# Performance work log

Hardware: AMD Instinct MI355X
Metric: run time of the kernel (lower is better)

## Reference

```python
import jax, jax.numpy as jnp
import numpy as np

B, T, F, C, L, W, NT, H = 4096, 64, 32, 64, 256, 512, 8, 12

# Tsit5 Butcher tableau (fixed-step, 6-stage FSAL-free form)
A21 = 0.161
A31, A32 = -0.008480655492356989, 0.335480655492357
A41, A42, A43 = 2.8971530571054935, -6.359448489975075, 4.362295432869581
A51, A52, A53, A54 = 5.325864828439257, -11.748883564062828, 7.4955393428898365, -0.09249506636175525
A61, A62, A63, A64, A65 = 5.86145544294642, -12.92096931784711, 8.159367898576159, -0.071584973281401, -0.028269050394068383
BC1, BC2, BC3, BC4, BC5, BC6 = 0.09646076681806523, 0.01, 0.4798896504144996, 1.379008574103742, -3.290069515436081, 2.324710524099774
SUBSTEPS = 10  # dt0 = 0.1, integrate each unit interval with 10 fixed steps


def setup_inputs() -> dict:
    key = jax.random.key(0)
    ks = jax.random.split(key, 16)
    def lin(k, out_d, in_d, scale=None):
        s = (1.0 / np.sqrt(in_d)) if scale is None else scale
        return jax.random.normal(k, (out_d, in_d), jnp.float32) * s
    inp = {
        "x_seq": jax.random.normal(ks[0], (B, T, F), jnp.float32),
        "country_idx": jax.random.randint(ks[1], (B,), 0, C),
        "horizon": H,
        # GRU encoder params (equinox GRUCell layout: 3*hidden stacked r,z,n)
        "W_ih": lin(ks[2], 3 * L, F + C),
        "W_hh": lin(ks[3], 3 * L, L),
        "b_ih": jnp.zeros((3 * L,), jnp.float32),
        "b_n": jnp.zeros((L,), jnp.float32),
        # NeuralField MLP 256->512->512->256, small init to keep the ODE stable
        "W0": lin(ks[4], W, L, 0.1 / np.sqrt(L)),
        "b0": jnp.zeros((W,), jnp.float32),
        "W1": lin(ks[5], W, W, 0.1 / np.sqrt(W)),
        "b1": jnp.zeros((W,), jnp.float32),
        "W2": lin(ks[6], L, W, 0.1 / np.sqrt(W)),
        "b2": jnp.zeros((L,), jnp.float32),
        # Decoder
        "W_dec": lin(ks[7], NT, L),
        "b_dec": jnp.zeros((NT,), jnp.float32),
    }
    return inp


def reference(x_seq, W_ih, W_hh, b_ih, b_n, W0, b0, W1, b1, W2, b2, W_dec, b_dec, country_idx, horizon):
    dtype = x_seq.dtype
    n_countries = W_ih.shape[1] - x_seq.shape[2]
    n_latent = W_hh.shape[1]
    ohe = jax.nn.one_hot(country_idx, n_countries, dtype=dtype)  # [B, C]

    # ---- GRU encoder scan over time ----
    h0 = jnp.zeros((x_seq.shape[0], n_latent), dtype)
    def gru_step(h, x_t):
        x_in = jnp.concatenate([x_t, ohe], axis=-1)          # [B, F+C]
        ih = x_in @ W_ih.T + b_ih                            # [B, 3L]
        hh = h @ W_hh.T                                      # [B, 3L]
        ir, iz, inn = jnp.split(ih, 3, axis=-1)
        hr, hz, hn = jnp.split(hh, 3, axis=-1)
        r = jax.nn.sigmoid(ir + hr)
        z = jax.nn.sigmoid(iz + hz)
        n = jnp.tanh(inn + r * (hn + b_n))
        return n + z * (h - n), None
    h_final, _ = jax.lax.scan(gru_step, h0, jnp.swapaxes(x_seq, 0, 1))

    # ---- Neural ODE vector field (autonomous ELU MLP) ----
    def f(y):
        a = jax.nn.elu(y @ W0.T + b0)
        a = jax.nn.elu(a @ W1.T + b1)
        return a @ W2.T + b2

    dt = jnp.asarray(1.0 / SUBSTEPS, dtype)
    def tsit5_step(y, _):
        k1 = f(y)
        k2 = f(y + dt * (A21 * k1))
        k3 = f(y + dt * (A31 * k1 + A32 * k2))
        k4 = f(y + dt * (A41 * k1 + A42 * k2 + A43 * k3))
        k5 = f(y + dt * (A51 * k1 + A52 * k2 + A53 * k3 + A54 * k4))
        k6 = f(y + dt * (A61 * k1 + A62 * k2 + A63 * k3 + A64 * k4 + A65 * k5))
        y_new = y + dt * (BC1 * k1 + BC2 * k2 + BC3 * k3 + BC4 * k4 + BC5 * k5 + BC6 * k6)
        return y_new, None

    def unit(y, _):
        y, _ = jax.lax.scan(tsit5_step, y, None, length=SUBSTEPS)
        return y, y  # save state at each integer time t = 1..horizon

    _, ys = jax.lax.scan(unit, h_final, None, length=horizon)  # [H, B, L]

    # ---- linear decode ----
    out = jnp.einsum('hbl,tl->bht', ys, W_dec) + b_dec  # [B, H, n_targets]
    return out
```

## Files before the change

### kernel.cpp

```cpp
#include <hip/hip_runtime.h>

typedef __bf16 bf16;
typedef __bf16 bf16x8 __attribute__((ext_vector_type(8)));
typedef __bf16 bf16x4 __attribute__((ext_vector_type(4)));
typedef float  f32x4  __attribute__((ext_vector_type(4)));
typedef unsigned int u32;

#define B_TOT 4096
#define T_SEQ 64
#define NT_OUT 8
#define NTHR 512
#define NBLK 256
#define GSZ  8

#define WS_W0   0
#define WS_W1   262144
#define WS_W2   786432
#define WS_WHH  1048576
#define WS_WIH  1441792
#define WS_BC   1490944
#define WS_GY   1703936
#define WS_GYB  3801088
#define WS_GH1  5898240
#define WS_GH2  10092544
#define WS_FLG  14286848
#define WS_MAP  14290944

constexpr float A21 = 0.161f;
constexpr float A31 = -0.008480655492356989f, A32 = 0.335480655492357f;
constexpr float A41 = 2.8971530571054935f, A42 = -6.359448489975075f, A43 = 4.362295432869581f;
constexpr float A51 = 5.325864828439257f, A52 = -11.748883564062828f, A53 = 7.4955393428898365f, A54 = -0.09249506636175525f;
constexpr float A61 = 5.86145544294642f, A62 = -12.92096931784711f, A63 = 8.159367898576159f, A64 = -0.071584973281401f, A65 = -0.028269050394068383f;
constexpr float BC1 = 0.09646076681806523f, BC2 = 0.01f, BC3 = 0.4798896504144996f;
constexpr float BC4 = 1.379008574103742f, BC5 = -3.290069515436081f, BC6 = 2.324710524099774f;
constexpr float DT = 0.1f;
constexpr float BROW[5][5] = {
    {A21, 0, 0, 0, 0},
    {A31, A32, 0, 0, 0},
    {A41, A42, A43, 0, 0},
    {A51, A52, A53, A54, 0},
    {A61, A62, A63, A64, A65}};
constexpr float FCF[6] = {BC1, BC2, BC3, BC4, BC5, BC6};

__device__ __forceinline__ f32x4 MFMA(bf16x8 a, bf16x8 b, f32x4 c) {
    return __builtin_amdgcn_mfma_f32_16x16x32_bf16(a, b, c, 0, 0, 0);
}
__device__ __forceinline__ float eluf(float x) { return x > 0.f ? x : __expf(x) - 1.f; }
__device__ __forceinline__ float sigm_f(float x) { return 1.f / (1.f + __expf(-x)); }
__device__ __forceinline__ float tanh_f(float x) { return 1.f - 2.f / (__expf(2.f * x) + 1.f); }

template<bool FAST>
__device__ __forceinline__ void ld4g(const bf16* p, bf16x8& a0, bf16x8& a1, bf16x8& a2, bf16x8& a3) {
    if constexpr (FAST) {
        asm volatile(
            "global_load_dwordx4 %0, %4, off sc0\n\t"
            "global_load_dwordx4 %1, %4, off offset:1024 sc0\n\t"
            "global_load_dwordx4 %2, %4, off offset:2048 sc0\n\t"
            "global_load_dwordx4 %3, %4, off offset:3072 sc0"
            : "=&v"(a0), "=&v"(a1), "=&v"(a2), "=&v"(a3) : "v"(p) : "memory");
    } else {
        asm volatile(
            "global_load_dwordx4 %0, %4, off sc0 sc1\n\t"
            "global_load_dwordx4 %1, %4, off offset:1024 sc0 sc1\n\t"
            "global_load_dwordx4 %2, %4, off offset:2048 sc0 sc1\n\t"
            "global_load_dwordx4 %3, %4, off offset:3072 sc0 sc1"
            : "=&v"(a0), "=&v"(a1), "=&v"(a2), "=&v"(a3) : "v"(p) : "memory");
    }
}
template<bool FAST>
__device__ __forceinline__ bf16x8 ld1g(const bf16* p) {
    bf16x8 a;
    if constexpr (FAST)
        asm volatile("global_load_dwordx4 %0, %1, off sc0\n\ts_waitcnt vmcnt(0)"
                     : "=v"(a) : "v"(p) : "memory");
    else
        asm volatile("global_load_dwordx4 %0, %1, off sc0 sc1\n\ts_waitcnt vmcnt(0)"
                     : "=v"(a) : "v"(p) : "memory");
    return a;
}
template<bool FAST>
__device__ __forceinline__ void st4g(bf16* p, bf16x4 v) {
    if constexpr (FAST) *(bf16x4*)p = v;
    else asm volatile("global_store_dwordx2 %0, %1, off sc0 sc1" :: "v"(p), "v"(v) : "memory");
}
__device__ __forceinline__ void vmwait() {
    asm volatile("s_waitcnt vmcnt(0)" ::: "memory");
    __builtin_amdgcn_sched_barrier(0);
}

__device__ __forceinline__ void produce(u32* f, int tid) {
    asm volatile("s_waitcnt vmcnt(0)" ::: "memory");
    __syncthreads();
    if (tid == 0) __hip_atomic_fetch_add(f, 1u, __ATOMIC_RELAXED, __HIP_MEMORY_SCOPE_AGENT);
}
__device__ __forceinline__ void consume(const u32* f, u32 tgt, int tid) {
    if (tid == 0) {
        while (__hip_atomic_load(f, __ATOMIC_RELAXED, __HIP_MEMORY_SCOPE_AGENT) < tgt)
            __builtin_amdgcn_s_sleep(1);
    }
    __syncthreads();
}

template<int ST, bool FAST>
__device__ __forceinline__ void ode_stage(
    const bf16* sW0, const bf16* sW1, const bf16* sW2,
    bf16* gY, bf16* gH1, bf16* gH2,
    u32* fY, u32* fH1, u32* fH2, int tid, int w, int lane,
    const f32x4 (&b0v)[4], const f32x4 (&b1v)[4], const f32x4 (&b2v)[2],
    const int (&dA)[4], const int (&dY)[2],
    f32x4 (&yreg)[2], f32x4 (&kreg)[5][2],
    u32& eY, u32& eH1, u32& eH2) {
    const f32x4 Z = {0.f, 0.f, 0.f, 0.f};
    {
        bf16x8 a[8];
        const bf16* p = gY + w * 4096 + lane * 8;
        ld4g<FAST>(p, a[0], a[1], a[2], a[3]);
        ld4g<FAST>(p + 2048, a[4], a[5], a[6], a[7]);
        vmwait();
        f32x4 acc[4] = {Z, Z, Z, Z};
        #pragma unroll
        for (int kk = 0; kk < 8; ++kk)
            #pragma unroll
            for (int nt = 0; nt < 4; ++nt)
                acc[nt] = MFMA(*(const bf16x8*)&sW0[(nt * 8 + kk) * 512 + lane * 8], a[kk], acc[nt]);
        #pragma unroll
        for (int nt = 0; nt < 4; ++nt) {
            bf16x4 ov;
            #pragma unroll
            for (int r = 0; r < 4; ++r) ov[r] = (bf16)eluf(acc[nt][r] + b0v[nt][r]);
            st4g<FAST>(gH1 + w * 8192 + dA[nt], ov);
        }
    }
    produce(fH1, tid); ++eH1;
    consume(fH1, GSZ * eH1, tid);
    {
        bf16x8 a[16];
        const bf16* p = gH1 + w * 8192 + lane * 8;
        ld4g<FAST>(p, a[0], a[1], a[2], a[3]);
        ld4g<FAST>(p + 2048, a[4], a[5], a[6], a[7]);
        ld4g<FAST>(p + 4096, a[8], a[9], a[10], a[11]);
        ld4g<FAST>(p + 6144, a[12], a[13], a[14], a[15]);
        vmwait();
        f32x4 acc[4] = {Z, Z, Z, Z};
        #pragma unroll
        for (int kk = 0; kk < 16; ++kk)
            #pragma unroll
            for (int nt = 0; nt < 4; ++nt)
                acc[nt] = MFMA(*(const bf16x8*)&sW1[(nt * 16 + kk) * 512 + lane * 8], a[kk], acc[nt]);
        #pragma unroll
        for (int nt = 0; nt < 4; ++nt) {
            bf16x4 ov;
            #pragma unroll
            for (int r = 0; r < 4; ++r) ov[r] = (bf16)eluf(acc[nt][r] + b1v[nt][r]);
            st4g<FAST>(gH2 + w * 8192 + dA[nt], ov);
        }
    }
    produce(fH2, tid); ++eH2;
    consume(fH2, GSZ * eH2, tid);
    {
        bf16x8 a[16];
        const bf16* p = gH2 + w * 8192 + lane * 8;
        ld4g<FAST>(p, a[0], a[1], a[2], a[3]);
        ld4g<FAST>(p + 2048, a[4], a[5], a[6], a[7]);
        ld4g<FAST>(p + 4096, a[8], a[9], a[10], a[11]);
        ld4g<FAST>(p + 6144, a[12], a[13], a[14], a[15]);
        vmwait();
        f32x4 acc[2] = {Z, Z};
        #pragma unroll
        for (int kk = 0; kk < 16; ++kk)
            #pragma unroll
            for (int nt = 0; nt < 2; ++nt)
                acc[nt] = MFMA(*(const bf16x8*)&sW2[(nt * 16 + kk) * 512 + lane * 8], a[kk], acc[nt]);
        #pragma unroll
        for (int nt = 0; nt < 2; ++nt) {
            f32x4 kv;
            #pragma unroll
            for (int r = 0; r < 4; ++r) kv[r] = acc[nt][r] + b2v[nt][r];
            f32x4 yst;
            if constexpr (ST < 5) {
                kreg[ST][nt] = kv;
                yst = yreg[nt];
                #pragma unroll
                for (int s = 0; s <= ST; ++s) {
                    const float c = DT * BROW[ST][s];
                    #pragma unroll
                    for (int r = 0; r < 4; ++r) yst[r] += c * kreg[s][nt][r];
                }
            } else {
                #pragma unroll
                for (int s = 0; s < 5; ++s) {
                    const float c = DT * FCF[s];
                    #pragma unroll
                    for (int r = 0; r < 4; ++r) yreg[nt][r] += c * kreg[s][nt][r];
                }
                #pragma unroll
                for (int r = 0; r < 4; ++r) yreg[nt][r] += (DT * FCF[5]) * kv[r];
                yst = yreg[nt];
            }
            bf16x4 ov;
            #pragma unroll
            for (int r = 0; r < 4; ++r) ov[r] = (bf16)yst[r];
            st4g<FAST>(gY + w * 4096 + dY[nt], ov);
        }
    }
    produce(fY, tid); ++eY;
}

template<bool FAST>
__device__ __forceinline__ void dec_unit(const bf16* gY, const float* sWdec, const float* sBdec,
                                         float* out, int g, int j, int w, int lane, int H, int u) {
    const int rloc = 2 * w + (lane >> 5);
    const int li = lane & 31;
    const bf16* p = gY + (size_t)j * 4096 + (((li >> 2) * 64 + (li & 3) * 16 + rloc)) * 8;
    bf16x8 yv = ld1g<FAST>(p);
    const int f0 = li * 8;
    float acc[8];
    #pragma unroll
    for (int t = 0; t < 8; ++t) acc[t] = 0.f;
    #pragma unroll
    for (int e = 0; e < 8; ++e) {
        const float yf = (float)yv[e];
        #pragma unroll
        for (int t = 0; t < 8; ++t) acc[t] += yf * sWdec[t * 256 + f0 + e];
    }
    #pragma unroll
    for (int k = 1; k < 32; k <<= 1)
        #pragma unroll
        for (int t = 0; t < 8; ++t) acc[t] += __shfl_xor(acc[t], k, 64);
    if (li == 0) {
        const size_t row = (size_t)g * 128 + 16 * j + rloc;
        #pragma unroll
        for (int t = 0; t < 8; ++t) out[(row * H + u) * NT_OUT + t] = acc[t] + sBdec[t];
    }
}

template<bool FAST>
__device__ void body(const float* __restrict__ x_seq, const int* __restrict__ cidx,
                     const float* __restrict__ b_n, const float* __restrict__ b0,
                     const float* __restrict__ b1, const float* __restrict__ b2,
                     const float* __restrict__ W_dec, const float* __restrict__ b_dec,
                     char* __restrict__ ws, float* __restrict__ out,
                     bf16* sWgt, float* sWdec, float* sBdec,
                     int H, int g, int j) {
    const int tid = threadIdx.x, w = tid >> 6, lane = tid & 63;
    const int lm = lane & 15, q = lane >> 4, q4 = q << 2;
    const int grow0 = g * 128;

    const bf16* W0p  = (const bf16*)(ws + WS_W0);
    const bf16* W1p  = (const bf16*)(ws + WS_W1);
    const bf16* W2p  = (const bf16*)(ws + WS_W2);
    const bf16* WhhP = (const bf16*)(ws + WS_WHH);
    const bf16* WihP = (const bf16*)(ws + WS_WIH);
    const float* bias_c = (const float*)(ws + WS_BC);
    bf16* gY  = (bf16*)(ws + WS_GY)  + (size_t)g * 32768;
    bf16* gYb = (bf16*)(ws + WS_GYB) + (size_t)g * 32768;
    bf16* gH1 = (bf16*)(ws + WS_GH1) + (size_t)g * 65536;
    bf16* gH2 = (bf16*)(ws + WS_GH2) + (size_t)g * 65536;
    u32* fl  = (u32*)(ws + WS_FLG + (size_t)g * 128);
    u32 *fY = fl, *fH1 = fl + 16, *fH2 = fl + 32;

    u32 eY = 0, eH1 = 0, eH2 = 0;

    for (int i = tid; i < 2048; i += NTHR) sWdec[i] = W_dec[i];
    if (tid < 8) sBdec[tid] = b_dec[tid];
    for (int i = tid; i < 54 * 64; i += NTHR) {
        const int fr = i >> 6, l = i & 63;
        const int tau = fr / 9, kk = fr % 9;
        const int gam = tau >> 1, p = tau & 1;
        const int c = gam * 16 + 2 * j + p;
        const bf16* src = (kk < 8) ? &WhhP[(((size_t)c) * 8 + kk) * 512 + l * 8]
                                   : &WihP[((size_t)c) * 512 + l * 8];
        *(bf16x8*)&sWgt[((size_t)fr) * 512 + l * 8] = *(const bf16x8*)src;
    }

    const int m = w;
    float bcr[2][4], bcz[2][4], bcn[2][4], bnr[2][4];
    {
        const int c = cidx[grow0 + 16 * m + lm];
        #pragma unroll
        for (int p = 0; p < 2; ++p)
            #pragma unroll
            for (int r = 0; r < 4; ++r) {
                const int F = 32 * j + p * 16 + q4 + r;
                bcr[p][r] = bias_c[(size_t)c * 768 + F];
                bcz[p][r] = bias_c[(size_t)c * 768 + 256 + F];
                bcn[p][r] = bias_c[(size_t)c * 768 + 512 + F];
                bnr[p][r] = b_n[F];
            }
    }
    int dY[2];
    #pragma unroll
    for (int p = 0; p < 2; ++p)
        dY[p] = (j * 64 + ((4 * j + 2 * p + (q >> 1)) & 3) * 16 + lm) * 8 + (q & 1) * 4;

    {
        bf16x4 z4;
        #pragma unroll
        for (int r = 0; r < 4; ++r) z4[r] = (bf16)0.f;
        st4g<FAST>(gY + m * 4096 + dY[0], z4);
        st4g<FAST>(gY + m * 4096 + dY[1], z4);
    }
    produce(fY, tid); ++eY;

    f32x4 hreg[2] = {{0.f, 0.f, 0.f, 0.f}, {0.f, 0.f, 0.f, 0.f}};
    const f32x4 Z = {0.f, 0.f, 0.f, 0.f};
    for (int t = 0; t < T_SEQ; ++t) {
        bf16x8 ax;
        {
            const float* xp = x_seq + (((size_t)(grow0 + 16 * m + lm)) * T_SEQ + t) * 32 + q * 8;
            f32x4 xa = *(const f32x4*)xp;
            f32x4 xb = *(const f32x4*)(xp + 4);
            #pragma unroll
            for (int e = 0; e < 4; ++e) { ax[e] = (bf16)xa[e]; ax[4 + e] = (bf16)xb[e]; }
        }
        consume(fY, GSZ * eY, tid);
        const bf16* hs = ((t & 1) ? gYb : gY) + m * 4096 + lane * 8;
        bf16x8 a[8];
        ld4g<FAST>(hs, a[0], a[1], a[2], a[3]);
        ld4g<FAST>(hs + 2048, a[4], a[5], a[6], a[7]);
        vmwait();
        f32x4 rz[4] = {Z, Z, Z, Z}, nH[2] = {Z, Z}, nX[2] = {Z, Z};
        #pragma unroll
        for (int kk = 0; kk < 8; ++kk) {
            #pragma unroll
            for (int p = 0; p < 2; ++p) {
                rz[p]     = MFMA(*(const bf16x8*)&sWgt[((0 + p) * 9 + kk) * 512 + lane * 8], a[kk], rz[p]);
                rz[2 + p] = MFMA(*(const bf16x8*)&sWgt[((2 + p) * 9 + kk) * 512 + lane * 8], a[kk], rz[2 + p]);
                nH[p]     = MFMA(*(const bf16x8*)&sWgt[((4 + p) * 9 + kk) * 512 + lane * 8], a[kk], nH[p]);
            }
        }
        #pragma unroll
        for (int p = 0; p < 2; ++p) {
            rz[p]     = MFMA(*(const bf16x8*)&sWgt[((0 + p) * 9 + 8) * 512 + lane * 8], ax, rz[p]);
            rz[2 + p] = MFMA(*(const bf16x8*)&sWgt[((2 + p) * 9 + 8) * 512 + lane * 8], ax, rz[2 + p]);
            nX[p]     = MFMA(*(const bf16x8*)&sWgt[((4 + p) * 9 + 8) * 512 + lane * 8], ax, nX[p]);
        }
        bf16* hd = (((t + 1) & 1) ? gYb : gY) + m * 4096;
        #pragma unroll
        for (int p = 0; p < 2; ++p) {
            bf16x4 ov;
            #pragma unroll
            for (int r = 0; r < 4; ++r) {
                const float rg = sigm_f(rz[p][r] + bcr[p][r]);
                const float zg = sigm_f(rz[2 + p][r] + bcz[p][r]);
                const float nn = tanh_f(nX[p][r] + bcn[p][r] + rg * (nH[p][r] + bnr[p][r]));
                hreg[p][r] = nn + zg * (hreg[p][r] - nn);
                ov[r] = (bf16)hreg[p][r];
            }
            st4g<FAST>(hd + dY[p], ov);
        }
        produce(fY, tid); ++eY;
    }

    bf16* sW0 = sWgt;
    bf16* sW1 = sWgt + 16384;
    bf16* sW2 = sWgt + 49152;
    for (int i = tid; i < 2048; i += NTHR)
        *(bf16x8*)&sW0[i * 8] = *(const bf16x8*)&W0p[(size_t)j * 16384 + i * 8];
    for (int i = tid; i < 4096; i += NTHR)
        *(bf16x8*)&sW1[i * 8] = *(const bf16x8*)&W1p[(size_t)j * 32768 + i * 8];
    for (int i = tid; i < 2048; i += NTHR)
        *(bf16x8*)&sW2[i * 8] = *(const bf16x8*)&W2p[(size_t)j * 16384 + i * 8];
    __syncthreads();

    f32x4 b0v[4], b1v[4], b2v[2];
    #pragma unroll
    for (int nt = 0; nt < 4; ++nt) {
        b0v[nt] = *(const f32x4*)&b0[64 * j + nt * 16 + q4];
        b1v[nt] = *(const f32x4*)&b1[64 * j + nt * 16 + q4];
    }
    #pragma unroll
    for (int nt = 0; nt < 2; ++nt) b2v[nt] = *(const f32x4*)&b2[32 * j + nt * 16 + q4];
    int dA[4];
    #pragma unroll
    for (int nt = 0; nt < 4; ++nt)
        dA[nt] = ((2 * j + (nt >> 1)) * 64 + ((8 * j + 2 * nt + (q >> 1)) & 3) * 16 + lm) * 8 + (q & 1) * 4;

    f32x4 yreg[2] = {hreg[0], hreg[1]};
    f32x4 kreg[5][2];

    const int NSS = H * 10;
    for (int ss = 0; ss < NSS; ++ss) {
        consume(fY, GSZ * eY, tid);
        if (ss && ss % 10 == 0)
            dec_unit<FAST>(gY, sWdec, sBdec, out, g, j, w, lane, H, ss / 10 - 1);
        ode_stage<0, FAST>(sW0, sW1, sW2, gY, gH1, gH2, fY, fH1, fH2, tid, w, lane,
                           b0v, b1v, b2v, dA, dY, yreg, kreg, eY, eH1, eH2);
        consume(fY, GSZ * eY, tid);
        ode_stage<1, FAST>(sW0, sW1, sW2, gY, gH1, gH2, fY, fH1, fH2, tid, w, lane,
                           b0v, b1v, b2v, dA, dY, yreg, kreg, eY, eH1, eH2);
        consume(fY, GSZ * eY, tid);
        ode_stage<2, FAST>(sW0, sW1, sW2, gY, gH1, gH2, fY, fH1, fH2, tid, w, lane,
                           b0v, b1v, b2v, dA, dY, yreg, kreg, eY, eH1, eH2);
        consume(fY, GSZ * eY, tid);
        ode_stage<3, FAST>(sW0, sW1, sW2, gY, gH1, gH2, fY, fH1, fH2, tid, w, lane,
                           b0v, b1v, b2v, dA, dY, yreg, kreg, eY, eH1, eH2);
        consume(fY, GSZ * eY, tid);
        ode_stage<4, FAST>(sW0, sW1, sW2, gY, gH1, gH2, fY, fH1, fH2, tid, w, lane,
                           b0v, b1v, b2v, dA, dY, yreg, kreg, eY, eH1, eH2);
        consume(fY, GSZ * eY, tid);
        ode_stage<5, FAST>(sW0, sW1, sW2, gY, gH1, gH2, fY, fH1, fH2, tid, w, lane,
                           b0v, b1v, b2v, dA, dY, yreg, kreg, eY, eH1, eH2);
    }
    consume(fY, GSZ * eY, tid);
    dec_unit<FAST>(gY, sWdec, sBdec, out, g, j, w, lane, H, H - 1);
}

__global__ void __launch_bounds__(NTHR, 2)
k_main(const float* __restrict__ x_seq, const int* __restrict__ cidx,
       const float* __restrict__ b_n, const float* __restrict__ b0,
       const float* __restrict__ b1, const float* __restrict__ b2,
       const float* __restrict__ W_dec, const float* __restrict__ b_dec,
       char* __restrict__ ws, float* __restrict__ out, int H) {
    __shared__ __align__(16) bf16 sWgt[65536];
    __shared__ __align__(16) float sWdec[2048];
    __shared__ float sBdec[8];
    __shared__ u32 mapL[NBLK];
    __shared__ int sMeta[3];

    const int tid = threadIdx.x, b = blockIdx.x;

    u32* xmap = (u32*)(ws + WS_MAP);
    u32* gctr = (u32*)(ws + WS_MAP + 1024);
    u32 xcc;
    asm volatile("s_getreg_b32 %0, hwreg(HW_REG_XCC_ID)" : "=s"(xcc));
    if (tid == 0) {
        __hip_atomic_store(&xmap[b], xcc, __ATOMIC_RELEASE, __HIP_MEMORY_SCOPE_AGENT);
        __hip_atomic_fetch_add(gctr, 1u, __ATOMIC_ACQ_REL, __HIP_MEMORY_SCOPE_AGENT);
        while (__hip_atomic_load(gctr, __ATOMIC_ACQUIRE, __HIP_MEMORY_SCOPE_AGENT) < NBLK)
            __builtin_amdgcn_s_sleep(8);
    }
    __syncthreads();
    if (tid < NBLK)
        mapL[tid] = __hip_atomic_load(&xmap[tid], __ATOMIC_ACQUIRE, __HIP_MEMORY_SCOPE_AGENT);
    __syncthreads();

    if (tid == 0) {
        int cnt[8] = {0, 0, 0, 0, 0, 0, 0, 0};
        int rank = 0, bad = 0;
        const u32 my = mapL[b];
        for (int i = 0; i < NBLK; ++i) {
            const u32 x = mapL[i];
            if (x > 7u) bad = 1;
            else cnt[x]++;
            if (i < b && x == my) ++rank;
        }
        int ok = !bad;
        #pragma unroll
        for (int i = 0; i < 8; ++i) ok &= (cnt[i] == 32);
        sMeta[0] = ok;
        sMeta[1] = ok ? (int)(my * 4 + (rank >> 3)) : ((b & 7) * 4 + (b >> 6));
        sMeta[2] = ok ? (rank & 7) : ((b >> 3) & 7);
    }
    __syncthreads();
    const int ok = sMeta[0], g = sMeta[1], j = sMeta[2];
    __syncthreads();

    if (ok)
        body<true>(x_seq, cidx, b_n, b0, b1, b2, W_dec, b_dec, ws, out,
                   sWgt, sWdec, sBdec, H, g, j);
    else
        body<false>(x_seq, cidx, b_n, b0, b1, b2, W_dec, b_dec, ws, out,
                    sWgt, sWdec, sBdec, H, g, j);
}

__global__ void k_pack(const float* __restrict__ src, bf16* __restrict__ dst,
                       int OUT, int K, int Ksrc, int koff) {
    const int total = (OUT * K) >> 3;
    for (int gg = blockIdx.x * blockDim.x + threadIdx.x; gg < total; gg += gridDim.x * blockDim.x) {
        const int lane = gg & 63, f = gg >> 6;
        const int KK = K >> 5;
        const int kk = f % KK, c = f / KK;
        const int col = c * 16 + (lane & 15);
        const int k0 = kk * 32 + ((lane >> 4) << 3);
        bf16x8 o;
        #pragma unroll
        for (int jj = 0; jj < 8; ++jj) o[jj] = (bf16)src[(size_t)col * Ksrc + koff + k0 + jj];
        *(bf16x8*)&dst[(size_t)gg * 8] = o;
    }
}

__global__ void k_bias(const float* __restrict__ W_ih, const float* __restrict__ b_ih,
                       float* __restrict__ bias_c) {
    const int i = blockIdx.x * blockDim.x + threadIdx.x;
    if (i < 64 * 768) {
        const int c = i / 768, n = i - c * 768;
        bias_c[i] = W_ih[(size_t)n * 96 + 32 + c] + b_ih[n];
    }
}

extern "C" void kernel_launch(void* const* d_in, const int* in_sizes, int n_in,
                              void* d_out, int out_size, void* d_ws, size_t ws_size,
                              hipStream_t stream) {
    const float* x_seq = (const float*)d_in[0];
    const int*   cidx  = (const int*)d_in[1];
    const float* W_ih  = (const float*)d_in[3];
    const float* W_hh  = (const float*)d_in[4];
    const float* b_ih  = (const float*)d_in[5];
    const float* b_n   = (const float*)d_in[6];
    const float* W0    = (const float*)d_in[7];
    const float* b0    = (const float*)d_in[8];
    const float* W1    = (const float*)d_in[9];
    const float* b1    = (const float*)d_in[10];
    const float* W2    = (const float*)d_in[11];
    const float* b2    = (const float*)d_in[12];
    const float* W_dec = (const float*)d_in[13];
    const float* b_dec = (const float*)d_in[14];
    float* out = (float*)d_out;
    const int H = out_size / (B_TOT * NT_OUT);
    char* ws = (char*)d_ws;

    hipMemsetAsync(ws + WS_FLG, 0, 8192, stream);

    k_pack<<<64, 256, 0, stream>>>(W0, (bf16*)(ws + WS_W0), 512, 256, 256, 0);
    k_pack<<<128, 256, 0, stream>>>(W1, (bf16*)(ws + WS_W1), 512, 512, 512, 0);
    k_pack<<<64, 256, 0, stream>>>(W2, (bf16*)(ws + WS_W2), 256, 512, 512, 0);
    k_pack<<<96, 256, 0, stream>>>(W_hh, (bf16*)(ws + WS_WHH), 768, 256, 256, 0);
    k_pack<<<12, 256, 0, stream>>>(W_ih, (bf16*)(ws + WS_WIH), 768, 32, 96, 0);
    k_bias<<<(64 * 768 + 255) / 256, 256, 0, stream>>>(W_ih, b_ih, (float*)(ws + WS_BC));

    k_main<<<NBLK, NTHR, 0, stream>>>(x_seq, cidx, b_n, b0, b1, b2, W_dec, b_dec,
                                      ws, out, H);
}
```

Measured before the change: 6.384 ms.

## Split each batch group across 16 blocks instead of 8, halving per-block work

Doubles the grid to 512 blocks and the group size to 16, so each block owns half as many output features per layer and holds half the weights in LDS. Occupancy is raised to 4 blocks per CU through the launch bounds. The consume wait is also changed so every thread spins on the flag itself, removing a __syncthreads. In exchange, each barrier now waits on twice as many producers and there is more flag polling traffic across the device.

```diff
diff --git a/kernel.cpp b/kernel.cpp
--- a/kernel.cpp
+++ b/kernel.cpp
@@ -10,8 +10,8 @@
 #define T_SEQ 64
 #define NT_OUT 8
 #define NTHR 512
-#define NBLK 256
-#define GSZ  8
+#define NBLK 512
+#define GSZ  16
 
 #define WS_W0   0
 #define WS_W1   262144
@@ -24,7 +24,7 @@
 #define WS_GH1  5898240
 #define WS_GH2  10092544
 #define WS_FLG  14286848
-#define WS_MAP  14290944
+#define WS_MAP  14295040
 
 constexpr float A21 = 0.161f;
 constexpr float A31 = -0.008480655492356989f, A32 = 0.335480655492357f;
@@ -93,12 +93,9 @@
     __syncthreads();
     if (tid == 0) __hip_atomic_fetch_add(f, 1u, __ATOMIC_RELAXED, __HIP_MEMORY_SCOPE_AGENT);
 }
-__device__ __forceinline__ void consume(const u32* f, u32 tgt, int tid) {
-    if (tid == 0) {
-        while (__hip_atomic_load(f, __ATOMIC_RELAXED, __HIP_MEMORY_SCOPE_AGENT) < tgt)
-            __builtin_amdgcn_s_sleep(1);
-    }
-    __syncthreads();
+__device__ __forceinline__ void consume(const u32* f, u32 tgt) {
+    while (__hip_atomic_load(f, __ATOMIC_RELAXED, __HIP_MEMORY_SCOPE_AGENT) < tgt)
+        __builtin_amdgcn_s_sleep(1);
 }
 
 template<int ST, bool FAST>
@@ -106,9 +103,9 @@
     const bf16* sW0, const bf16* sW1, const bf16* sW2,
     bf16* gY, bf16* gH1, bf16* gH2,
     u32* fY, u32* fH1, u32* fH2, int tid, int w, int lane,
-    const f32x4 (&b0v)[4], const f32x4 (&b1v)[4], const f32x4 (&b2v)[2],
-    const int (&dA)[4], const int (&dY)[2],
-    f32x4 (&yreg)[2], f32x4 (&kreg)[5][2],
+    const f32x4 (&b0v)[2], const f32x4 (&b1v)[2], const f32x4& b2v,
+    const int (&dA)[2], int dY,
+    f32x4& yreg, f32x4 (&kreg)[5],
     u32& eY, u32& eH1, u32& eH2) {
     const f32x4 Z = {0.f, 0.f, 0.f, 0.f};
     {
@@ -117,14 +114,14 @@
         ld4g<FAST>(p, a[0], a[1], a[2], a[3]);
         ld4g<FAST>(p + 2048, a[4], a[5], a[6], a[7]);
         vmwait();
-        f32x4 acc[4] = {Z, Z, Z, Z};
+        f32x4 acc[2] = {Z, Z};
         #pragma unroll
         for (int kk = 0; kk < 8; ++kk)
             #pragma unroll
-            for (int nt = 0; nt < 4; ++nt)
+            for (int nt = 0; nt < 2; ++nt)
                 acc[nt] = MFMA(*(const bf16x8*)&sW0[(nt * 8 + kk) * 512 + lane * 8], a[kk], acc[nt]);
         #pragma unroll
-        for (int nt = 0; nt < 4; ++nt) {
+        for (int nt = 0; nt < 2; ++nt) {
             bf16x4 ov;
             #pragma unroll
             for (int r = 0; r < 4; ++r) ov[r] = (bf16)eluf(acc[nt][r] + b0v[nt][r]);
@@ -132,7 +129,7 @@
         }
     }
     produce(fH1, tid); ++eH1;
-    consume(fH1, GSZ * eH1, tid);
+    consume(fH1, GSZ * eH1);
     {
         bf16x8 a[16];
         const bf16* p = gH1 + w * 8192 + lane * 8;
@@ -141,14 +138,14 @@
         ld4g<FAST>(p + 4096, a[8], a[9], a[10], a[11]);
         ld4g<FAST>(p + 6144, a[12], a[13], a[14], a[15]);
         vmwait();
-        f32x4 acc[4] = {Z, Z, Z, Z};
+        f32x4 acc[2] = {Z, Z};
         #pragma unroll
         for (int kk = 0; kk < 16; ++kk)
             #pragma unroll
-            for (int nt = 0; nt < 4; ++nt)
+            for (int nt = 0; nt < 2; ++nt)
                 acc[nt] = MFMA(*(const bf16x8*)&sW1[(nt * 16 + kk) * 512 + lane * 8], a[kk], acc[nt]);
         #pragma unroll
-        for (int nt = 0; nt < 4; ++nt) {
+        for (int nt = 0; nt < 2; ++nt) {
             bf16x4 ov;
             #pragma unroll
             for (int r = 0; r < 4; ++r) ov[r] = (bf16)eluf(acc[nt][r] + b1v[nt][r]);
@@ -156,7 +153,7 @@
         }
     }
     produce(fH2, tid); ++eH2;
-    consume(fH2, GSZ * eH2, tid);
+    consume(fH2, GSZ * eH2);
     {
         bf16x8 a[16];
         const bf16* p = gH2 + w * 8192 + lane * 8;
@@ -165,43 +162,38 @@
         ld4g<FAST>(p + 4096, a[8], a[9], a[10], a[11]);
         ld4g<FAST>(p + 6144, a[12], a[13], a[14], a[15]);
         vmwait();
-        f32x4 acc[2] = {Z, Z};
+        f32x4 acc = {0.f, 0.f, 0.f, 0.f};
         #pragma unroll
         for (int kk = 0; kk < 16; ++kk)
-            #pragma unroll
-            for (int nt = 0; nt < 2; ++nt)
-                acc[nt] = MFMA(*(const bf16x8*)&sW2[(nt * 16 + kk) * 512 + lane * 8], a[kk], acc[nt]);
-        #pragma unroll
-        for (int nt = 0; nt < 2; ++nt) {
-            f32x4 kv;
-            #pragma unroll
-            for (int r = 0; r < 4; ++r) kv[r] = acc[nt][r] + b2v[nt][r];
-            f32x4 yst;
-            if constexpr (ST < 5) {
-                kreg[ST][nt] = kv;
-                yst = yreg[nt];
+            acc = MFMA(*(const bf16x8*)&sW2[kk * 512 + lane * 8], a[kk], acc);
+        f32x4 kv;
+        #pragma unroll
+        for (int r = 0; r < 4; ++r) kv[r] = acc[r] + b2v[r];
+        f32x4 yst;
+        if constexpr (ST < 5) {
+            kreg[ST] = kv;
+            yst = yreg;
+            #pragma unroll
+            for (int s = 0; s <= ST; ++s) {
+                const float c = DT * BROW[ST][s];
                 #pragma unroll
-                for (int s = 0; s <= ST; ++s) {
-                    const float c = DT * BROW[ST][s];
-                    #pragma unroll
-                    for (int r = 0; r < 4; ++r) yst[r] += c * kreg[s][nt][r];
-                }
-            } else {
+                for (int r = 0; r < 4; ++r) yst[r] += c * kreg[s][r];
+            }
+        } else {
+            #pragma unroll
+            for (int s = 0; s < 5; ++s) {
+                const float c = DT * FCF[s];
                 #pragma unroll
-                for (int s = 0; s < 5; ++s) {
-                    const float c = DT * FCF[s];
-                    #pragma unroll
-                    for (int r = 0; r < 4; ++r) yreg[nt][r] += c * kreg[s][nt][r];
-                }
-                #pragma unroll
-                for (int r = 0; r < 4; ++r) yreg[nt][r] += (DT * FCF[5]) * kv[r];
-                yst = yreg[nt];
+                for (int r = 0; r < 4; ++r) yreg[r] += c * kreg[s][r];
             }
-            bf16x4 ov;
-            #pragma unroll
-            for (int r = 0; r < 4; ++r) ov[r] = (bf16)yst[r];
-            st4g<FAST>(gY + w * 4096 + dY[nt], ov);
-        }
+            #pragma unroll
+            for (int r = 0; r < 4; ++r) yreg[r] += (DT * FCF[5]) * kv[r];
+            yst = yreg;
+        }
+        bf16x4 ov;
+        #pragma unroll
+        for (int r = 0; r < 4; ++r) ov[r] = (bf16)yst[r];
+        st4g<FAST>(gY + w * 4096 + dY, ov);
     }
     produce(fY, tid); ++eY;
 }
@@ -209,9 +201,9 @@
 template<bool FAST>
 __device__ __forceinline__ void dec_unit(const bf16* gY, const float* sWdec, const float* sBdec,
                                          float* out, int g, int j, int w, int lane, int H, int u) {
-    const int rloc = 2 * w + (lane >> 5);
+    const int rt = (j & 1) * 8 + w;
     const int li = lane & 31;
-    const bf16* p = gY + (size_t)j * 4096 + (((li >> 2) * 64 + (li & 3) * 16 + rloc)) * 8;
+    const bf16* p = gY + (size_t)(j >> 1) * 4096 + ((li >> 2) * 64 + (li & 3) * 16 + rt) * 8;
     bf16x8 yv = ld1g<FAST>(p);
     const int f0 = li * 8;
     float acc[8];
@@ -227,8 +219,8 @@
     for (int k = 1; k < 32; k <<= 1)
         #pragma unroll
         for (int t = 0; t < 8; ++t) acc[t] += __shfl_xor(acc[t], k, 64);
-    if (li == 0) {
-        const size_t row = (size_t)g * 128 + 16 * j + rloc;
+    if (lane == 0) {
+        const size_t row = (size_t)g * 128 + (j >> 1) * 16 + rt;
         #pragma unroll
         for (int t = 0; t < 8; ++t) out[(row * H + u) * NT_OUT + t] = acc[t] + sBdec[t];
     }
@@ -256,53 +248,46 @@
     bf16* gYb = (bf16*)(ws + WS_GYB) + (size_t)g * 32768;
     bf16* gH1 = (bf16*)(ws + WS_GH1) + (size_t)g * 65536;
     bf16* gH2 = (bf16*)(ws + WS_GH2) + (size_t)g * 65536;
-    u32* fl  = (u32*)(ws + WS_FLG + (size_t)g * 128);
+    u32* fl  = (u32*)(ws + WS_FLG + (size_t)g * 256);
     u32 *fY = fl, *fH1 = fl + 16, *fH2 = fl + 32;
 
     u32 eY = 0, eH1 = 0, eH2 = 0;
 
     for (int i = tid; i < 2048; i += NTHR) sWdec[i] = W_dec[i];
     if (tid < 8) sBdec[tid] = b_dec[tid];
-    for (int i = tid; i < 54 * 64; i += NTHR) {
+    for (int i = tid; i < 27 * 64; i += NTHR) {
         const int fr = i >> 6, l = i & 63;
-        const int tau = fr / 9, kk = fr % 9;
-        const int gam = tau >> 1, p = tau & 1;
-        const int c = gam * 16 + 2 * j + p;
+        const int gam = fr / 9, kk = fr % 9;
+        const int c = gam * 16 + j;
         const bf16* src = (kk < 8) ? &WhhP[(((size_t)c) * 8 + kk) * 512 + l * 8]
                                    : &WihP[((size_t)c) * 512 + l * 8];
         *(bf16x8*)&sWgt[((size_t)fr) * 512 + l * 8] = *(const bf16x8*)src;
     }
 
     const int m = w;
-    float bcr[2][4], bcz[2][4], bcn[2][4], bnr[2][4];
+    float bcr[4], bcz[4], bcn[4], bnr[4];
     {
         const int c = cidx[grow0 + 16 * m + lm];
         #pragma unroll
-        for (int p = 0; p < 2; ++p)
-            #pragma unroll
-            for (int r = 0; r < 4; ++r) {
-                const int F = 32 * j + p * 16 + q4 + r;
-                bcr[p][r] = bias_c[(size_t)c * 768 + F];
-                bcz[p][r] = bias_c[(size_t)c * 768 + 256 + F];
-                bcn[p][r] = bias_c[(size_t)c * 768 + 512 + F];
-                bnr[p][r] = b_n[F];
-            }
-    }
-    int dY[2];
-    #pragma unroll
-    for (int p = 0; p < 2; ++p)
-        dY[p] = (j * 64 + ((4 * j + 2 * p + (q >> 1)) & 3) * 16 + lm) * 8 + (q & 1) * 4;
+        for (int r = 0; r < 4; ++r) {
+            const int F = 16 * j + q4 + r;
+            bcr[r] = bias_c[(size_t)c * 768 + F];
+            bcz[r] = bias_c[(size_t)c * 768 + 256 + F];
+            bcn[r] = bias_c[(size_t)c * 768 + 512 + F];
+            bnr[r] = b_n[F];
+        }
+    }
+    const int dY = ((j >> 1) * 64 + (lm | (((2 * j + (q >> 1)) & 3) << 4))) * 8 + (q & 1) * 4;
 
     {
         bf16x4 z4;
         #pragma unroll
         for (int r = 0; r < 4; ++r) z4[r] = (bf16)0.f;
-        st4g<FAST>(gY + m * 4096 + dY[0], z4);
-        st4g<FAST>(gY + m * 4096 + dY[1], z4);
+        st4g<FAST>(gY + m * 4096 + dY, z4);
     }
     produce(fY, tid); ++eY;
 
-    f32x4 hreg[2] = {{0.f, 0.f, 0.f, 0.f}, {0.f, 0.f, 0.f, 0.f}};
+    f32x4 hreg = {0.f, 0.f, 0.f, 0.f};
     const f32x4 Z = {0.f, 0.f, 0.f, 0.f};
     for (int t = 0; t < T_SEQ; ++t) {
         bf16x8 ax;
@@ -313,106 +298,96 @@
             #pragma unroll
             for (int e = 0; e < 4; ++e) { ax[e] = (bf16)xa[e]; ax[4 + e] = (bf16)xb[e]; }
         }
-        consume(fY, GSZ * eY, tid);
+        consume(fY, GSZ * eY);
         const bf16* hs = ((t & 1) ? gYb : gY) + m * 4096 + lane * 8;
         bf16x8 a[8];
         ld4g<FAST>(hs, a[0], a[1], a[2], a[3]);
         ld4g<FAST>(hs + 2048, a[4], a[5], a[6], a[7]);
         vmwait();
-        f32x4 rz[4] = {Z, Z, Z, Z}, nH[2] = {Z, Z}, nX[2] = {Z, Z};
+        f32x4 aR = Z, aZ = Z, aNH = Z, aNX = Z;
         #pragma unroll
         for (int kk = 0; kk < 8; ++kk) {
-            #pragma unroll
-            for (int p = 0; p < 2; ++p) {
-                rz[p]     = MFMA(*(const bf16x8*)&sWgt[((0 + p) * 9 + kk) * 512 + lane * 8], a[kk], rz[p]);
-                rz[2 + p] = MFMA(*(const bf16x8*)&sWgt[((2 + p) * 9 + kk) * 512 + lane * 8], a[kk], rz[2 + p]);
-                nH[p]     = MFMA(*(const bf16x8*)&sWgt[((4 + p) * 9 + kk) * 512 + lane * 8], a[kk], nH[p]);
-            }
-        }
-        #pragma unroll
-        for (int p = 0; p < 2; ++p) {
-            rz[p]     = MFMA(*(const bf16x8*)&sWgt[((0 + p) * 9 + 8) * 512 + lane * 8], ax, rz[p]);
-            rz[2 + p] = MFMA(*(const bf16x8*)&sWgt[((2 + p) * 9 + 8) * 512 + lane * 8], ax, rz[2 + p]);
-            nX[p]     = MFMA(*(const bf16x8*)&sWgt[((4 + p) * 9 + 8) * 512 + lane * 8], ax, nX[p]);
-        }
+            aR  = MFMA(*(const bf16x8*)&sWgt[(0 * 9 + kk) * 512 + lane * 8], a[kk], aR);
+            aZ  = MFMA(*(const bf16x8*)&sWgt[(1 * 9 + kk) * 512 + lane * 8], a[kk], aZ);
+            aNH = MFMA(*(const bf16x8*)&sWgt[(2 * 9 + kk) * 512 + lane * 8], a[kk], aNH);
+        }
+        aR  = MFMA(*(const bf16x8*)&sWgt[(0 * 9 + 8) * 512 + lane * 8], ax, aR);
+        aZ  = MFMA(*(const bf16x8*)&sWgt[(1 * 9 + 8) * 512 + lane * 8], ax, aZ);
+        aNX = MFMA(*(const bf16x8*)&sWgt[(2 * 9 + 8) * 512 + lane * 8], ax, aNX);
         bf16* hd = (((t + 1) & 1) ? gYb : gY) + m * 4096;
-        #pragma unroll
-        for (int p = 0; p < 2; ++p) {
-            bf16x4 ov;
-            #pragma unroll
-            for (int r = 0; r < 4; ++r) {
-                const float rg = sigm_f(rz[p][r] + bcr[p][r]);
-                const float zg = sigm_f(rz[2 + p][r] + bcz[p][r]);
-                const float nn = tanh_f(nX[p][r] + bcn[p][r] + rg * (nH[p][r] + bnr[p][r]));
-                hreg[p][r] = nn + zg * (hreg[p][r] - nn);
-                ov[r] = (bf16)hreg[p][r];
-            }
-            st4g<FAST>(hd + dY[p], ov);
-        }
+        bf16x4 ov;
+        #pragma unroll
+        for (int r = 0; r < 4; ++r) {
+            const float rg = sigm_f(aR[r] + bcr[r]);
+            const float zg = sigm_f(aZ[r] + bcz[r]);
+            const float nn = tanh_f(aNX[r] + bcn[r] + rg * (aNH[r] + bnr[r]));
+            hreg[r] = nn + zg * (hreg[r] - nn);
+            ov[r] = (bf16)hreg[r];
+        }
+        st4g<FAST>(hd + dY, ov);
         produce(fY, tid); ++eY;
     }
 
     bf16* sW0 = sWgt;
-    bf16* sW1 = sWgt + 16384;
-    bf16* sW2 = sWgt + 49152;
+    bf16* sW1 = sWgt + 8192;
+    bf16* sW2 = sWgt + 24576;
+    for (int i = tid; i < 1024; i += NTHR)
+        *(bf16x8*)&sW0[i * 8] = *(const bf16x8*)&W0p[(size_t)j * 8192 + i * 8];
     for (int i = tid; i < 2048; i += NTHR)
-        *(bf16x8*)&sW0[i * 8] = *(const bf16x8*)&W0p[(size_t)j * 16384 + i * 8];
-    for (int i = tid; i < 4096; i += NTHR)
-        *(bf16x8*)&sW1[i * 8] = *(const bf16x8*)&W1p[(size_t)j * 32768 + i * 8];
-    for (int i = tid; i < 2048; i += NTHR)
-        *(bf16x8*)&sW2[i * 8] = *(const bf16x8*)&W2p[(size_t)j * 16384 + i * 8];
-    __syncthreads();
-
-    f32x4 b0v[4], b1v[4], b2v[2];
+        *(bf16x8*)&sW1[i * 8] = *(const bf16x8*)&W1p[(size_t)j * 16384 + i * 8];
+    for (int i = tid; i < 1024; i += NTHR)
+        *(bf16x8*)&sW2[i * 8] = *(const bf16x8*)&W2p[(size_t)j * 8192 + i * 8];
+    __syncthreads();
+
+    f32x4 b0v[2], b1v[2];
     #pragma unroll
-    for (int nt = 0; nt < 4; ++nt) {
-        b0v[nt] = *(const f32x4*)&b0[64 * j + nt * 16 + q4];
-        b1v[nt] = *(const f32x4*)&b1[64 * j + nt * 16 + q4];
-    }
+    for (int nt = 0; nt < 2; ++nt) {
+        b0v[nt] = *(const f32x4*)&b0[32 * j + nt * 16 + q4];
+        b1v[nt] = *(const f32x4*)&b1[32 * j + nt * 16 + q4];
+    }
+    const f32x4 b2v = *(const f32x4*)&b2[16 * j + q4];
+    int dA[2];
     #pragma unroll
-    for (int nt = 0; nt < 2; ++nt) b2v[nt] = *(const f32x4*)&b2[32 * j + nt * 16 + q4];
-    int dA[4];
-    #pragma unroll
-    for (int nt = 0; nt < 4; ++nt)
-        dA[nt] = ((2 * j + (nt >> 1)) * 64 + ((8 * j + 2 * nt + (q >> 1)) & 3) * 16 + lm) * 8 + (q & 1) * 4;
-
-    f32x4 yreg[2] = {hreg[0], hreg[1]};
-    f32x4 kreg[5][2];
+    for (int nt = 0; nt < 2; ++nt)
+        dA[nt] = (j * 64 + (lm | (((4 * j + 2 * nt + (q >> 1)) & 3) << 4))) * 8 + (q & 1) * 4;
+
+    f32x4 yreg = hreg;
+    f32x4 kreg[5];
 
     const int NSS = H * 10;
     for (int ss = 0; ss < NSS; ++ss) {
-        consume(fY, GSZ * eY, tid);
+        consume(fY, GSZ * eY);
         if (ss && ss % 10 == 0)
             dec_unit<FAST>(gY, sWdec, sBdec, out, g, j, w, lane, H, ss / 10 - 1);
         ode_stage<0, FAST>(sW0, sW1, sW2, gY, gH1, gH2, fY, fH1, fH2, tid, w, lane,
                            b0v, b1v, b2v, dA, dY, yreg, kreg, eY, eH1, eH2);
-        consume(fY, GSZ * eY, tid);
+        consume(fY, GSZ * eY);
         ode_stage<1, FAST>(sW0, sW1, sW2, gY, gH1, gH2, fY, fH1, fH2, tid, w, lane,
                            b0v, b1v, b2v, dA, dY, yreg, kreg, eY, eH1, eH2);
-        consume(fY, GSZ * eY, tid);
+        consume(fY, GSZ * eY);
         ode_stage<2, FAST>(sW0, sW1, sW2, gY, gH1, gH2, fY, fH1, fH2, tid, w, lane,
                            b0v, b1v, b2v, dA, dY, yreg, kreg, eY, eH1, eH2);
-        consume(fY, GSZ * eY, tid);
+        consume(fY, GSZ * eY);
         ode_stage<3, FAST>(sW0, sW1, sW2, gY, gH1, gH2, fY, fH1, fH2, tid, w, lane,
                            b0v, b1v, b2v, dA, dY, yreg, kreg, eY, eH1, eH2);
-        consume(fY, GSZ * eY, tid);
+        consume(fY, GSZ * eY);
         ode_stage<4, FAST>(sW0, sW1, sW2, gY, gH1, gH2, fY, fH1, fH2, tid, w, lane,
                            b0v, b1v, b2v, dA, dY, yreg, kreg, eY, eH1, eH2);
-        consume(fY, GSZ * eY, tid);
+        consume(fY, GSZ * eY);
         ode_stage<5, FAST>(sW0, sW1, sW2, gY, gH1, gH2, fY, fH1, fH2, tid, w, lane,
                            b0v, b1v, b2v, dA, dY, yreg, kreg, eY, eH1, eH2);
     }
-    consume(fY, GSZ * eY, tid);
+    consume(fY, GSZ * eY);
     dec_unit<FAST>(gY, sWdec, sBdec, out, g, j, w, lane, H, H - 1);
 }
 
-__global__ void __launch_bounds__(NTHR, 2)
+__global__ void __launch_bounds__(NTHR, 4)
 k_main(const float* __restrict__ x_seq, const int* __restrict__ cidx,
        const float* __restrict__ b_n, const float* __restrict__ b0,
        const float* __restrict__ b1, const float* __restrict__ b2,
        const float* __restrict__ W_dec, const float* __restrict__ b_dec,
        char* __restrict__ ws, float* __restrict__ out, int H) {
-    __shared__ __align__(16) bf16 sWgt[65536];
+    __shared__ __align__(16) bf16 sWgt[32768];
     __shared__ __align__(16) float sWdec[2048];
     __shared__ float sBdec[8];
     __shared__ u32 mapL[NBLK];
@@ -421,7 +396,7 @@
     const int tid = threadIdx.x, b = blockIdx.x;
 
     u32* xmap = (u32*)(ws + WS_MAP);
-    u32* gctr = (u32*)(ws + WS_MAP + 1024);
+    u32* gctr = (u32*)(ws + WS_MAP + 2048);
     u32 xcc;
     asm volatile("s_getreg_b32 %0, hwreg(HW_REG_XCC_ID)" : "=s"(xcc));
     if (tid == 0) {
@@ -447,10 +422,10 @@
         }
         int ok = !bad;
         #pragma unroll
-        for (int i = 0; i < 8; ++i) ok &= (cnt[i] == 32);
+        for (int i = 0; i < 8; ++i) ok &= (cnt[i] == 64);
         sMeta[0] = ok;
-        sMeta[1] = ok ? (int)(my * 4 + (rank >> 3)) : ((b & 7) * 4 + (b >> 6));
-        sMeta[2] = ok ? (rank & 7) : ((b >> 3) & 7);
+        sMeta[1] = ok ? (int)(my * 4 + (rank & 3)) : (b >> 4);
+        sMeta[2] = ok ? (rank >> 2) : (b & 15);
     }
     __syncthreads();
     const int ok = sMeta[0], g = sMeta[1], j = sMeta[2];
@@ -510,7 +485,7 @@
     const int H = out_size / (B_TOT * NT_OUT);
     char* ws = (char*)d_ws;
 
-    hipMemsetAsync(ws + WS_FLG, 0, 8192, stream);
+    hipMemsetAsync(ws + WS_FLG, 0, 16384, stream);
 
     k_pack<<<64, 256, 0, stream>>>(W0, (bf16*)(ws + WS_W0), 512, 256, 256, 0);
     k_pack<<<128, 256, 0, stream>>>(W1, (bf16*)(ws + WS_W1), 512, 512, 512, 0);
```

After: 20.08 ms. 3.14x slower.
